# Optimization experiments

Measured on AMD Instinct MI355X. Metric: run time of the kernel, lower is better.

The kernel has to match this reference:

```python
import jax, jax.numpy as jnp
import numpy as np

# 14 MZI blocks on 6 modes (0-indexed), fixed circuit topology from the module
MODES = [[0, 1], [4, 5], [1, 2], [3, 4]] + [[0, 1], [2, 3], [4, 5], [1, 2], [3, 4]] * 2
IN_CONFIG = (0, 3)  # two input photons in modes 0 and 3
OUT_PAIRS = [(i, j) for i in range(6) for j in range(i + 1, 6)]  # 15 distinct output configs
BATCH = 262144
EPS = 1e-12  # F.normalize eps


def setup_inputs() -> dict:
    key = jax.random.key(0)
    k1, k2, k3 = jax.random.split(key, 3)
    return {
        "x": jax.random.normal(k1, (BATCH, 12), dtype=jnp.float32),
        "param_phi": 0.1 * jax.random.normal(k2, (4,), dtype=jnp.float32),
        "param_theta": 0.1 * jax.random.normal(k3, (8,), dtype=jnp.float32),
        "input_k": jnp.ones((12,), dtype=jnp.float32),
        "input_b": jnp.zeros((12,), dtype=jnp.float32),
    }


def reference(x, param_phi, param_theta, input_k, input_b):
    B = x.shape[0]
    xs = x * input_k + input_b  # [B, 12]
    bc = lambda v: jnp.broadcast_to(v, (B, v.shape[0]))
    # Assemble per-sample theta/phi lists exactly as get_batch_ansatz does
    theta = jnp.concatenate(
        [bc(param_theta[0:4]), xs[:, 3:6], bc(param_theta[4:6]), xs[:, 9:12], bc(param_theta[6:8])], axis=1
    )  # [B, 14]
    phi = jnp.concatenate(
        [jnp.zeros((B, 4), x.dtype), xs[:, 0:3], bc(param_phi[0:2]), xs[:, 6:9], bc(param_phi[2:4])], axis=1
    )  # [B, 14]

    # Build 6x6 unitary per sample as a product of 2x2 Givens/MZI blocks:
    # T = [[e^{i phi} cos t, -sin t], [e^{i phi} sin t, cos t]] acting on rows (i, j)
    U = jnp.broadcast_to(jnp.eye(6, dtype=jnp.complex64), (B, 6, 6))
    for k, (i, j) in enumerate(MODES):
        t, p = theta[:, k], phi[:, k]
        ep = jnp.exp(1j * p)  # complex64
        ct = jnp.cos(t).astype(jnp.complex64)
        st = jnp.sin(t).astype(jnp.complex64)
        ri, rj = U[:, i, :], U[:, j, :]
        new_i = (ep * ct)[:, None] * ri - st[:, None] * rj
        new_j = (ep * st)[:, None] * ri + ct[:, None] * rj
        U = U.at[:, i, :].set(new_i).at[:, j, :].set(new_j)

    # Boson sampling amplitudes for 2 photons: permanent of 2x2 submatrix U[out_rows, in_cols]
    A = U[:, :, jnp.array(IN_CONFIG)]  # [B, 6, 2]
    oa = jnp.array([p[0] for p in OUT_PAIRS])
    ob = jnp.array([p[1] for p in OUT_PAIRS])
    amp = A[:, oa, 0] * A[:, ob, 1] + A[:, oa, 1] * A[:, ob, 0]  # [B, 15]

    # F.normalize(p=2, dim=1) for complex vectors, then torch.abs
    norm = jnp.sqrt(jnp.sum(jnp.abs(amp) ** 2, axis=1, keepdims=True))
    amp = amp / jnp.maximum(norm, EPS)
    return jnp.abs(amp)
```

## Files before the change

### kernel.cpp

```cpp
#include <hip/hip_runtime.h>

#define BATCH 262144

struct C { float r, i; };

__device__ __forceinline__ void rotp(C& u, C& v, float ct, float st, float cp, float sp) {
    float ar = cp * ct, ai = sp * ct;
    float br = cp * st, bi = sp * st;
    C nu, nv;
    nu.r = ar * u.r - ai * u.i - st * v.r;
    nu.i = ar * u.i + ai * u.r - st * v.i;
    nv.r = br * u.r - bi * u.i + ct * v.r;
    nv.i = br * u.i + bi * u.r + ct * v.i;
    u = nu; v = nv;
}

__device__ __forceinline__ void rotr(C& u, C& v, float ct, float st) {
    C nu, nv;
    nu.r = ct * u.r - st * v.r;
    nu.i = ct * u.i - st * v.i;
    nv.r = st * u.r + ct * v.r;
    nv.i = st * u.i + ct * v.i;
    u = nu; v = nv;
}

__global__ __launch_bounds__(256) void bqnn_kernel(
    const float* __restrict__ x,
    const float* __restrict__ pphi,
    const float* __restrict__ pth,
    const float* __restrict__ ink,
    const float* __restrict__ inb,
    float* __restrict__ out) {
    __shared__ float ls[256 * 15];

    const int t = threadIdx.x;
    const int elem = blockIdx.x * 256 + t;

    const float4* x4 = reinterpret_cast<const float4*>(x) + (long long)elem * 3;
    float4 v0 = x4[0], v1 = x4[1], v2 = x4[2];

    const float xs0  = v0.x * ink[0]  + inb[0];
    const float xs1  = v0.y * ink[1]  + inb[1];
    const float xs2  = v0.z * ink[2]  + inb[2];
    const float xs3  = v0.w * ink[3]  + inb[3];
    const float xs4  = v1.x * ink[4]  + inb[4];
    const float xs5  = v1.y * ink[5]  + inb[5];
    const float xs6  = v1.z * ink[6]  + inb[6];
    const float xs7  = v1.w * ink[7]  + inb[7];
    const float xs8  = v2.x * ink[8]  + inb[8];
    const float xs9  = v2.y * ink[9]  + inb[9];
    const float xs10 = v2.z * ink[10] + inb[10];
    const float xs11 = v2.w * ink[11] + inb[11];

    C a0{1.f,0.f}, a1{0.f,0.f}, a2{0.f,0.f}, a3{0.f,0.f}, a4{0.f,0.f}, a5{0.f,0.f};
    C b0{0.f,0.f}, b1{0.f,0.f}, b2{0.f,0.f}, b3{1.f,0.f}, b4{0.f,0.f}, b5{0.f,0.f};

#define ROTR(I, J, TH) do { \
        float st_ = __sinf(TH), ct_ = __cosf(TH); \
        rotr(a##I, a##J, ct_, st_); \
        rotr(b##I, b##J, ct_, st_); \
    } while (0)

#define ROTP(I, J, TH, PH) do { \
        float st_ = __sinf(TH), ct_ = __cosf(TH); \
        float sp_ = __sinf(PH), cp_ = __cosf(PH); \
        rotp(a##I, a##J, ct_, st_, cp_, sp_); \
        rotp(b##I, b##J, ct_, st_, cp_, sp_); \
    } while (0)

    ROTR(0, 1, pth[0]);
    ROTR(4, 5, pth[1]);
    ROTR(1, 2, pth[2]);
    ROTR(3, 4, pth[3]);
    ROTP(0, 1, xs3,  xs0);
    ROTP(2, 3, xs4,  xs1);
    ROTP(4, 5, xs5,  xs2);
    ROTP(1, 2, pth[4], pphi[0]);
    ROTP(3, 4, pth[5], pphi[1]);
    ROTP(0, 1, xs9,  xs6);
    ROTP(2, 3, xs10, xs7);
    ROTP(4, 5, xs11, xs8);
    ROTP(1, 2, pth[6], pphi[2]);
    ROTP(3, 4, pth[7], pphi[3]);

#undef ROTR
#undef ROTP

#define PAIR(I, J, K) \
    { float re_ = a##I.r * b##J.r - a##I.i * b##J.i + a##J.r * b##I.r - a##J.i * b##I.i; \
      float im_ = a##I.r * b##J.i + a##I.i * b##J.r + a##J.r * b##I.i + a##J.i * b##I.r; \
      m##K = re_ * re_ + im_ * im_; s += m##K; }

    float m0,m1,m2,m3,m4,m5,m6,m7,m8,m9,m10,m11,m12,m13,m14;
    float s = 0.f;
    PAIR(0,1,0)  PAIR(0,2,1)  PAIR(0,3,2)  PAIR(0,4,3)  PAIR(0,5,4)
    PAIR(1,2,5)  PAIR(1,3,6)  PAIR(1,4,7)  PAIR(1,5,8)
    PAIR(2,3,9)  PAIR(2,4,10) PAIR(2,5,11)
    PAIR(3,4,12) PAIR(3,5,13)
    PAIR(4,5,14)
#undef PAIR

    float sc = fmaxf(s, 1e-24f);
    float invs = 1.f / sc;

    float* row = ls + t * 15;
    row[0]  = __fsqrt_rn(m0  * invs);
    row[1]  = __fsqrt_rn(m1  * invs);
    row[2]  = __fsqrt_rn(m2  * invs);
    row[3]  = __fsqrt_rn(m3  * invs);
    row[4]  = __fsqrt_rn(m4  * invs);
    row[5]  = __fsqrt_rn(m5  * invs);
    row[6]  = __fsqrt_rn(m6  * invs);
    row[7]  = __fsqrt_rn(m7  * invs);
    row[8]  = __fsqrt_rn(m8  * invs);
    row[9]  = __fsqrt_rn(m9  * invs);
    row[10] = __fsqrt_rn(m10 * invs);
    row[11] = __fsqrt_rn(m11 * invs);
    row[12] = __fsqrt_rn(m12 * invs);
    row[13] = __fsqrt_rn(m13 * invs);
    row[14] = __fsqrt_rn(m14 * invs);

    __syncthreads();

    float* oblk = out + (long long)blockIdx.x * (256 * 15);
    #pragma unroll
    for (int i = 0; i < 15; ++i) {
        int idx = i * 256 + t;
        oblk[idx] = ls[idx];
    }
}

extern "C" void kernel_launch(void* const* d_in, const int* in_sizes, int n_in,
                              void* d_out, int out_size, void* d_ws, size_t ws_size,
                              hipStream_t stream) {
    const float* x    = (const float*)d_in[0];
    const float* pphi = (const float*)d_in[1];
    const float* pth  = (const float*)d_in[2];
    const float* ink  = (const float*)d_in[3];
    const float* inb  = (const float*)d_in[4];
    float* out = (float*)d_out;

    bqnn_kernel<<<BATCH / 256, 256, 0, stream>>>(x, pphi, pth, ink, inb, out);
}
```

Baseline: 76.43 us.

## Process two elements per thread, hoist parameter trig, vectorize output stores

Each thread now handles two batch elements, so a block covers 512 samples and the grid is halved. The sin/cos of the shared parameters is computed once per thread and reused for both elements, rather than recomputed per element. The normalization uses the hardware reciprocal and sqrt builtins in place of correctly rounded ones, and the shared-memory staging is written back to global memory as float4. This costs twice the shared memory per block, which may lower occupancy, and slightly reduces numerical precision.

Measured after the change: 75.86 us. Within noise of the previous version (-0.7%).

```diff
diff --git a/kernel.cpp b/kernel.cpp
--- a/kernel.cpp
+++ b/kernel.cpp
@@ -24,67 +24,45 @@
     u = nu; v = nv;
 }
 
-__global__ __launch_bounds__(256) void bqnn_kernel(
-    const float* __restrict__ x,
-    const float* __restrict__ pphi,
-    const float* __restrict__ pth,
-    const float* __restrict__ ink,
-    const float* __restrict__ inb,
-    float* __restrict__ out) {
-    __shared__ float ls[256 * 15];
+struct UT {
+    float ct0, st0, ct1, st1, ct2, st2, ct3, st3;
+    float ct4, st4, cp0, sp0;
+    float ct5, st5, cp1, sp1;
+    float ct6, st6, cp2, sp2;
+    float ct7, st7, cp3, sp3;
+};
 
-    const int t = threadIdx.x;
-    const int elem = blockIdx.x * 256 + t;
-
-    const float4* x4 = reinterpret_cast<const float4*>(x) + (long long)elem * 3;
-    float4 v0 = x4[0], v1 = x4[1], v2 = x4[2];
-
-    const float xs0  = v0.x * ink[0]  + inb[0];
-    const float xs1  = v0.y * ink[1]  + inb[1];
-    const float xs2  = v0.z * ink[2]  + inb[2];
-    const float xs3  = v0.w * ink[3]  + inb[3];
-    const float xs4  = v1.x * ink[4]  + inb[4];
-    const float xs5  = v1.y * ink[5]  + inb[5];
-    const float xs6  = v1.z * ink[6]  + inb[6];
-    const float xs7  = v1.w * ink[7]  + inb[7];
-    const float xs8  = v2.x * ink[8]  + inb[8];
-    const float xs9  = v2.y * ink[9]  + inb[9];
-    const float xs10 = v2.z * ink[10] + inb[10];
-    const float xs11 = v2.w * ink[11] + inb[11];
-
-    C a0{1.f,0.f}, a1{0.f,0.f}, a2{0.f,0.f}, a3{0.f,0.f}, a4{0.f,0.f}, a5{0.f,0.f};
-    C b0{0.f,0.f}, b1{0.f,0.f}, b2{0.f,0.f}, b3{1.f,0.f}, b4{0.f,0.f}, b5{0.f,0.f};
-
-#define ROTR(I, J, TH) do { \
-        float st_ = __sinf(TH), ct_ = __cosf(TH); \
-        rotr(a##I, a##J, ct_, st_); \
-        rotr(b##I, b##J, ct_, st_); \
-    } while (0)
-
-#define ROTP(I, J, TH, PH) do { \
+#define ROTRU(I, J, CT, ST) do { rotr(a##I, a##J, CT, ST); rotr(b##I, b##J, CT, ST); } while (0)
+#define ROTPU(I, J, CT, ST, CP, SP) do { rotp(a##I, a##J, CT, ST, CP, SP); rotp(b##I, b##J, CT, ST, CP, SP); } while (0)
+#define ROTPD(I, J, TH, PH) do { \
         float st_ = __sinf(TH), ct_ = __cosf(TH); \
         float sp_ = __sinf(PH), cp_ = __cosf(PH); \
         rotp(a##I, a##J, ct_, st_, cp_, sp_); \
         rotp(b##I, b##J, ct_, st_, cp_, sp_); \
     } while (0)
 
-    ROTR(0, 1, pth[0]);
-    ROTR(4, 5, pth[1]);
-    ROTR(1, 2, pth[2]);
-    ROTR(3, 4, pth[3]);
-    ROTP(0, 1, xs3,  xs0);
-    ROTP(2, 3, xs4,  xs1);
-    ROTP(4, 5, xs5,  xs2);
-    ROTP(1, 2, pth[4], pphi[0]);
-    ROTP(3, 4, pth[5], pphi[1]);
-    ROTP(0, 1, xs9,  xs6);
-    ROTP(2, 3, xs10, xs7);
-    ROTP(4, 5, xs11, xs8);
-    ROTP(1, 2, pth[6], pphi[2]);
-    ROTP(3, 4, pth[7], pphi[3]);
+__device__ __forceinline__ void compute_elem(
+    float xs0, float xs1, float xs2, float xs3, float xs4, float xs5,
+    float xs6, float xs7, float xs8, float xs9, float xs10, float xs11,
+    const UT& u, float* __restrict__ row)
+{
+    C a0{1.f,0.f}, a1{0.f,0.f}, a2{0.f,0.f}, a3{0.f,0.f}, a4{0.f,0.f}, a5{0.f,0.f};
+    C b0{0.f,0.f}, b1{0.f,0.f}, b2{0.f,0.f}, b3{1.f,0.f}, b4{0.f,0.f}, b5{0.f,0.f};
 
-#undef ROTR
-#undef ROTP
+    ROTRU(0, 1, u.ct0, u.st0);
+    ROTRU(4, 5, u.ct1, u.st1);
+    ROTRU(1, 2, u.ct2, u.st2);
+    ROTRU(3, 4, u.ct3, u.st3);
+    ROTPD(0, 1, xs3,  xs0);
+    ROTPD(2, 3, xs4,  xs1);
+    ROTPD(4, 5, xs5,  xs2);
+    ROTPU(1, 2, u.ct4, u.st4, u.cp0, u.sp0);
+    ROTPU(3, 4, u.ct5, u.st5, u.cp1, u.sp1);
+    ROTPD(0, 1, xs9,  xs6);
+    ROTPD(2, 3, xs10, xs7);
+    ROTPD(4, 5, xs11, xs8);
+    ROTPU(1, 2, u.ct6, u.st6, u.cp2, u.sp2);
+    ROTPU(3, 4, u.ct7, u.st7, u.cp3, u.sp3);
 
 #define PAIR(I, J, K) \
     { float re_ = a##I.r * b##J.r - a##I.i * b##J.i + a##J.r * b##I.r - a##J.i * b##I.i; \
@@ -100,33 +78,80 @@
     PAIR(4,5,14)
 #undef PAIR
 
-    float sc = fmaxf(s, 1e-24f);
-    float invs = 1.f / sc;
+    float invs = __builtin_amdgcn_rcpf(fmaxf(s, 1e-24f));
+    row[0]  = __builtin_amdgcn_sqrtf(m0  * invs);
+    row[1]  = __builtin_amdgcn_sqrtf(m1  * invs);
+    row[2]  = __builtin_amdgcn_sqrtf(m2  * invs);
+    row[3]  = __builtin_amdgcn_sqrtf(m3  * invs);
+    row[4]  = __builtin_amdgcn_sqrtf(m4  * invs);
+    row[5]  = __builtin_amdgcn_sqrtf(m5  * invs);
+    row[6]  = __builtin_amdgcn_sqrtf(m6  * invs);
+    row[7]  = __builtin_amdgcn_sqrtf(m7  * invs);
+    row[8]  = __builtin_amdgcn_sqrtf(m8  * invs);
+    row[9]  = __builtin_amdgcn_sqrtf(m9  * invs);
+    row[10] = __builtin_amdgcn_sqrtf(m10 * invs);
+    row[11] = __builtin_amdgcn_sqrtf(m11 * invs);
+    row[12] = __builtin_amdgcn_sqrtf(m12 * invs);
+    row[13] = __builtin_amdgcn_sqrtf(m13 * invs);
+    row[14] = __builtin_amdgcn_sqrtf(m14 * invs);
+}
 
-    float* row = ls + t * 15;
-    row[0]  = __fsqrt_rn(m0  * invs);
-    row[1]  = __fsqrt_rn(m1  * invs);
-    row[2]  = __fsqrt_rn(m2  * invs);
-    row[3]  = __fsqrt_rn(m3  * invs);
-    row[4]  = __fsqrt_rn(m4  * invs);
-    row[5]  = __fsqrt_rn(m5  * invs);
-    row[6]  = __fsqrt_rn(m6  * invs);
-    row[7]  = __fsqrt_rn(m7  * invs);
-    row[8]  = __fsqrt_rn(m8  * invs);
-    row[9]  = __fsqrt_rn(m9  * invs);
-    row[10] = __fsqrt_rn(m10 * invs);
-    row[11] = __fsqrt_rn(m11 * invs);
-    row[12] = __fsqrt_rn(m12 * invs);
-    row[13] = __fsqrt_rn(m13 * invs);
-    row[14] = __fsqrt_rn(m14 * invs);
+__global__ __launch_bounds__(256) void bqnn_kernel(
+    const float* __restrict__ x,
+    const float* __restrict__ pphi,
+    const float* __restrict__ pth,
+    const float* __restrict__ ink,
+    const float* __restrict__ inb,
+    float* __restrict__ out) {
+    __shared__ alignas(16) float ls[512 * 15];
+
+    const int t = threadIdx.x;
+    const long long e0 = (long long)blockIdx.x * 512 + t;
+
+    const float4* x4 = reinterpret_cast<const float4*>(x);
+    float4 A0 = x4[e0 * 3 + 0], A1 = x4[e0 * 3 + 1], A2 = x4[e0 * 3 + 2];
+    float4 B0 = x4[(e0 + 256) * 3 + 0], B1 = x4[(e0 + 256) * 3 + 1], B2 = x4[(e0 + 256) * 3 + 2];
+
+    UT u;
+    u.ct0 = __cosf(pth[0]); u.st0 = __sinf(pth[0]);
+    u.ct1 = __cosf(pth[1]); u.st1 = __sinf(pth[1]);
+    u.ct2 = __cosf(pth[2]); u.st2 = __sinf(pth[2]);
+    u.ct3 = __cosf(pth[3]); u.st3 = __sinf(pth[3]);
+    u.ct4 = __cosf(pth[4]); u.st4 = __sinf(pth[4]);
+    u.ct5 = __cosf(pth[5]); u.st5 = __sinf(pth[5]);
+    u.ct6 = __cosf(pth[6]); u.st6 = __sinf(pth[6]);
+    u.ct7 = __cosf(pth[7]); u.st7 = __sinf(pth[7]);
+    u.cp0 = __cosf(pphi[0]); u.sp0 = __sinf(pphi[0]);
+    u.cp1 = __cosf(pphi[1]); u.sp1 = __sinf(pphi[1]);
+    u.cp2 = __cosf(pphi[2]); u.sp2 = __sinf(pphi[2]);
+    u.cp3 = __cosf(pphi[3]); u.sp3 = __sinf(pphi[3]);
+
+    const float k0=ink[0], k1=ink[1], k2=ink[2], k3=ink[3], k4=ink[4],  k5=ink[5];
+    const float k6=ink[6], k7=ink[7], k8=ink[8], k9=ink[9], k10=ink[10], k11=ink[11];
+    const float c0=inb[0], c1=inb[1], c2=inb[2], c3=inb[3], c4=inb[4],  c5=inb[5];
+    const float c6=inb[6], c7=inb[7], c8=inb[8], c9=inb[9], c10=inb[10], c11=inb[11];
+
+    compute_elem(A0.x*k0+c0, A0.y*k1+c1, A0.z*k2+c2, A0.w*k3+c3,
+                 A1.x*k4+c4, A1.y*k5+c5, A1.z*k6+c6, A1.w*k7+c7,
+                 A2.x*k8+c8, A2.y*k9+c9, A2.z*k10+c10, A2.w*k11+c11,
+                 u, ls + t * 15);
+    compute_elem(B0.x*k0+c0, B0.y*k1+c1, B0.z*k2+c2, B0.w*k3+c3,
+                 B1.x*k4+c4, B1.y*k5+c5, B1.z*k6+c6, B1.w*k7+c7,
+                 B2.x*k8+c8, B2.y*k9+c9, B2.z*k10+c10, B2.w*k11+c11,
+                 u, ls + (256 + t) * 15);
 
     __syncthreads();
 
-    float* oblk = out + (long long)blockIdx.x * (256 * 15);
+    float4* o4 = reinterpret_cast<float4*>(out) + (long long)blockIdx.x * 1920;
+    const float4* l4 = reinterpret_cast<const float4*>(ls);
     #pragma unroll
-    for (int i = 0; i < 15; ++i) {
+    for (int i = 0; i < 7; ++i) {
         int idx = i * 256 + t;
-        oblk[idx] = ls[idx];
+        o4[idx] = l4[idx];
+    }
+    if (t < 128) {
+        int idx = 1792 + t;
+        o4[idx] = l4[idx];
     }
 }
 
@@ -140,5 +165,5 @@
     const float* inb  = (const float*)d_in[4];
     float* out = (float*)d_out;
 
-    bqnn_kernel<<<BATCH / 256, 256, 0, stream>>>(x, pphi, pth, ink, inb, out);
+    bqnn_kernel<<<BATCH / 512, 256, 0, stream>>>(x, pphi, pth, ink, inb, out);
 }
```
